# Kernel tuning notes

Hardware: AMD Instinct MI355X
Metric: run time of the kernel (lower is better)

## Reference

```python
import jax, jax.numpy as jnp
import numpy as np

TOPK = 2
ALPHA_AUX = 0.02

def setup_inputs() -> dict:
    key = jax.random.key(0)
    ks = jax.random.split(key, 6)
    B, T, D, E, H = 2, 2048, 1024, 16, 1536
    s_in = 1.0 / np.sqrt(D)
    s_h = 1.0 / np.sqrt(H)
    return {
        "x": jax.random.normal(ks[0], (B, T, D), dtype=jnp.float32),
        "router_w": jax.random.normal(ks[1], (E, D), dtype=jnp.float32) * s_in,
        "w1": jax.random.normal(ks[2], (E, H, D), dtype=jnp.float32) * s_in,
        "b1": jax.random.normal(ks[3], (E, H), dtype=jnp.float32) * 0.01,
        "w2": jax.random.normal(ks[4], (E, D, H), dtype=jnp.float32) * s_h,
        "b2": jax.random.normal(ks[5], (E, D), dtype=jnp.float32) * 0.01,
    }

def reference(x, router_w, w1, b1, w2, b2):
    B, T, D = x.shape
    E = router_w.shape[0]
    N = B * T
    x_flat = x.reshape(N, D)

    # Router: top-k logits -> softmax gates -> dense dispatch matrix [N, E]
    logits = x_flat @ router_w.T                      # [N, E]
    vals, idx = jax.lax.top_k(logits, TOPK)           # [N, K]
    gate = jax.nn.softmax(vals, axis=-1)              # [N, K]
    rows = jnp.arange(N)[:, None]
    dispatch = jnp.zeros((N, E), dtype=x.dtype).at[rows, idx].set(gate)

    # Expert MLPs computed densely over all experts; gate==0 masks unselected,
    # reproducing the gather-MLP-scatter math exactly.
    h = jnp.einsum('nd,ehd->neh', x_flat, w1) + b1    # [N, E, H]
    h = jax.nn.gelu(h, approximate=True)              # tanh GELU
    y = jnp.einsum('neh,edh->ned', h, w2) + b2        # [N, E, D]
    out = jnp.einsum('ne,ned->nd', dispatch, y).reshape(B, T, D)

    # Auxiliary load-balancing loss
    tok_per_expert = (dispatch > 0).sum(0).astype(jnp.float32)  # [E]
    f_i = tok_per_expert / tok_per_expert.sum()
    m_i = dispatch.sum(0) / jnp.clip(tok_per_expert, 1.0, None)
    aux_loss = ALPHA_AUX * (f_i * m_i).mean()
    return out, aux_loss
```

## Files before the change

kernel.cpp:

```cpp
#include <hip/hip_runtime.h>
#include <hip/hip_bf16.h>
#include <math.h>

#define N_TOK 4096
#define DIM   1024
#define NEXP  16
#define HID   1536
#define TOPK2 2
#define NASSIGN (N_TOK * TOPK2)

#define MAX_ITEMS 80

typedef __attribute__((ext_vector_type(8))) short short8;
typedef __attribute__((ext_vector_type(4))) float floatx4;
typedef unsigned short u16;

#define GLOAD_LDS16(gp, lp)                                                     \
    __builtin_amdgcn_global_load_lds(                                           \
        (const __attribute__((address_space(1))) unsigned int*)(gp),            \
        (__attribute__((address_space(3))) unsigned int*)(lp), 16, 0, 0)

__global__ void cvt_kernel(const float* __restrict__ src, u16* __restrict__ dst, int n4) {
    int i = blockIdx.x * 256 + threadIdx.x;
    if (i >= n4) return;
    float4 v = ((const float4*)src)[i];
    __hip_bfloat16 a = __float2bfloat16(v.x), b = __float2bfloat16(v.y);
    __hip_bfloat16 c = __float2bfloat16(v.z), d = __float2bfloat16(v.w);
    ushort4 o;
    o.x = *(u16*)&a; o.y = *(u16*)&b; o.z = *(u16*)&c; o.w = *(u16*)&d;
    ((ushort4*)dst)[i] = o;
}

__global__ __launch_bounds__(256)
void logits_topk_kernel(const float* __restrict__ x, const float* __restrict__ rw,
                        int* __restrict__ idx, float* __restrict__ gate) {
    int tb = blockIdx.x * 16;
    __shared__ float xs[16][68];
    __shared__ float rs[16][68];
    __shared__ float lg[16][17];

    int tid = threadIdx.x;
    int t = tid >> 4, e = tid & 15;
    int srow = tid >> 4, scol = (tid & 15) * 4;

    float acc = 0.f;
    for (int k0 = 0; k0 < DIM; k0 += 64) {
        *(float4*)&xs[srow][scol] = *(const float4*)&x[(size_t)(tb + srow) * DIM + k0 + scol];
        *(float4*)&rs[srow][scol] = *(const float4*)&rw[(size_t)srow * DIM + k0 + scol];
        __syncthreads();
        const float2* xp = (const float2*)xs[t];
        const float2* rp = (const float2*)rs[e];
        #pragma unroll
        for (int k = 0; k < 32; k++) {
            float2 a = xp[k], b = rp[k];
            acc = fmaf(a.x, b.x, acc);
            acc = fmaf(a.y, b.y, acc);
        }
        __syncthreads();
    }
    lg[t][e] = acc;
    __syncthreads();

    if (tid < 16) {
        int n = tb + tid;
        float v0 = -3.402823466e+38f, v1 = -3.402823466e+38f;
        int i0 = 0, i1 = 0;
        #pragma unroll
        for (int ee = 0; ee < NEXP; ee++) {
            float v = lg[tid][ee];
            if (v > v0) { v1 = v0; i1 = i0; v0 = v; i0 = ee; }
            else if (v > v1) { v1 = v; i1 = ee; }
        }
        float e1 = expf(v1 - v0);
        float inv = 1.f / (1.f + e1);
        idx[2 * n] = i0; idx[2 * n + 1] = i1;
        gate[2 * n] = inv; gate[2 * n + 1] = e1 * inv;
    }
}

__global__ __launch_bounds__(256)
void plan_kernel(const int* __restrict__ idx, const float* __restrict__ gate,
                 int* __restrict__ offsets, int* __restrict__ tlist,
                 int* __restrict__ wl, int* __restrict__ wcount,
                 float* __restrict__ aux_out) {
    __shared__ int cnt_s[16];
    __shared__ float gs_s[16];
    __shared__ int pos_s[16];
    __shared__ int offs_s[17];
    int tid = threadIdx.x;
    if (tid < 16) { cnt_s[tid] = 0; gs_s[tid] = 0.f; pos_s[tid] = 0; }
    __syncthreads();
    for (int i = tid; i < NASSIGN; i += 256) {
        int e = idx[i];
        atomicAdd(&cnt_s[e], 1);
        atomicAdd(&gs_s[e], gate[i]);
    }
    __syncthreads();
    if (tid == 0) {
        int acc = 0;
        for (int e = 0; e < NEXP; e++) { offs_s[e] = acc; acc += cnt_s[e]; }
        offs_s[NEXP] = acc;
        float tot = (float)acc;
        float s = 0.f;
        for (int e = 0; e < NEXP; e++) {
            float c = (float)cnt_s[e];
            s += (c / tot) * (gs_s[e] / fmaxf(c, 1.f));
        }
        *aux_out = 0.02f * (s / (float)NEXP);
        int m = 0;
        for (int e = 0; e < NEXP; e++) {
            int nt = (cnt_s[e] + 127) >> 7;
            for (int rt = 0; rt < nt; rt++) wl[m++] = (e << 8) | rt;
        }
        *wcount = m;
    }
    __syncthreads();
    if (tid < 17) offsets[tid] = offs_s[tid];
    for (int i = tid; i < NASSIGN; i += 256) {
        int e = idx[i];
        int p = atomicAdd(&pos_s[e], 1);
        tlist[offs_s[e] + p] = i;
    }
}

__device__ __forceinline__ float gelu_tanh(float v) {
    float v3 = v * v * v;
    float t = tanhf(0.7978845608028654f * (v + 0.044715f * v3));
    return 0.5f * v * (1.f + t);
}


__global__ __launch_bounds__(256)
void gemm1_kernel(const u16* __restrict__ xb, const u16* __restrict__ w1b,
                  const float* __restrict__ b1,
                  const int* __restrict__ offsets, const int* __restrict__ tlist,
                  const int* __restrict__ wl, const int* __restrict__ wcount,
                  u16* __restrict__ h_bf) {
    int bid = blockIdx.x;
    int item = bid / 12;
    if (item >= *wcount) return;
    int colt = bid - item * 12;
    int w = wl[item];
    int e = w >> 8, rt = w & 255;
    int beg = offsets[e], ne = offsets[e + 1] - beg;
    int row0 = rt * 128, col0 = colt * 128;

    __shared__ u16 As[128 * 32];
    __shared__ u16 Bs[128 * 32];

    int tid = threadIdx.x;
    int wave = tid >> 6, lane = tid & 63;
    int wm = wave & 1, wn = wave >> 1;

    int koff = (((lane & 3) ^ ((lane >> 3) & 3)) * 8);
    const u16* aptr[2];
    const u16* bptr[2];
    #pragma unroll
    for (int q = 0; q < 2; q++) {
        int lrow = wave * 32 + q * 16 + (lane >> 2);
        int gi = beg + row0 + lrow;
        int gi2 = (row0 + lrow < ne) ? gi : beg;
        int tok = tlist[gi2] >> 1;
        aptr[q] = xb + (size_t)tok * DIM + koff;
        int n = col0 + lrow;
        bptr[q] = w1b + (size_t)(e * HID + n) * DIM + koff;
    }

    int rchunk = (((lane >> 4) ^ ((lane >> 1) & 3)) * 8);

    floatx4 acc[4][4] = {};
    for (int k0 = 0; k0 < DIM; k0 += 32) {
        #pragma unroll
        for (int q = 0; q < 2; q++) {
            GLOAD_LDS16(aptr[q] + k0, &As[(wave * 32 + q * 16) * 32]);
            GLOAD_LDS16(bptr[q] + k0, &Bs[(wave * 32 + q * 16) * 32]);
        }
        __syncthreads();
        short8 af[4], bf_[4];
        #pragma unroll
        for (int mi = 0; mi < 4; mi++)
            af[mi] = *(const short8*)&As[(wm * 64 + mi * 16 + (lane & 15)) * 32 + rchunk];
        #pragma unroll
        for (int nj = 0; nj < 4; nj++)
            bf_[nj] = *(const short8*)&Bs[(wn * 64 + nj * 16 + (lane & 15)) * 32 + rchunk];
        #pragma unroll
        for (int mi = 0; mi < 4; mi++)
            #pragma unroll
            for (int nj = 0; nj < 4; nj++)
                acc[mi][nj] = __builtin_amdgcn_mfma_f32_16x16x32_bf16(af[mi], bf_[nj], acc[mi][nj], 0, 0, 0);
        __syncthreads();
    }

    #pragma unroll
    for (int mi = 0; mi < 4; mi++) {
        #pragma unroll
        for (int r = 0; r < 4; r++) {
            int lrow = wm * 64 + mi * 16 + (lane >> 4) * 4 + r;
            if (row0 + lrow >= ne) continue;
            size_t orow = (size_t)(beg + row0 + lrow);
            #pragma unroll
            for (int nj = 0; nj < 4; nj++) {
                int col = col0 + wn * 64 + nj * 16 + (lane & 15);
                float v = acc[mi][nj][r] + b1[e * HID + col];
                __hip_bfloat16 hb = __float2bfloat16(gelu_tanh(v));
                h_bf[orow * HID + col] = *(u16*)&hb;
            }
        }
    }
}

__global__ __launch_bounds__(256)
void gemm2_kernel(const u16* __restrict__ h_bf, const u16* __restrict__ w2b,
                  const float* __restrict__ b2,
                  const int* __restrict__ offsets, const int* __restrict__ tlist,
                  const int* __restrict__ wl, const int* __restrict__ wcount,
                  const float* __restrict__ gate, float* __restrict__ out) {
    int bid = blockIdx.x;
    int item = bid >> 3;
    if (item >= *wcount) return;
    int colt = bid & 7;
    int w = wl[item];
    int e = w >> 8, rt = w & 255;
    int beg = offsets[e], ne = offsets[e + 1] - beg;
    int row0 = rt * 128, col0 = colt * 128;

    __shared__ u16 As[128 * 32];
    __shared__ u16 Bs[128 * 32];

    int tid = threadIdx.x;
    int wave = tid >> 6, lane = tid & 63;
    int wm = wave & 1, wn = wave >> 1;

    int koff = (((lane & 3) ^ ((lane >> 3) & 3)) * 8);
    const u16* aptr[2];
    const u16* bptr[2];
    #pragma unroll
    for (int q = 0; q < 2; q++) {
        int lrow = wave * 32 + q * 16 + (lane >> 2);
        int gi = beg + row0 + lrow;
        int gi2 = (row0 + lrow < ne) ? gi : beg;
        aptr[q] = h_bf + (size_t)gi2 * HID + koff;
        int n = col0 + lrow;
        bptr[q] = w2b + (size_t)(e * DIM + n) * HID + koff;
    }

    int rchunk = (((lane >> 4) ^ ((lane >> 1) & 3)) * 8);

    floatx4 acc[4][4] = {};
    for (int k0 = 0; k0 < HID; k0 += 32) {
        #pragma unroll
        for (int q = 0; q < 2; q++) {
            GLOAD_LDS16(aptr[q] + k0, &As[(wave * 32 + q * 16) * 32]);
            GLOAD_LDS16(bptr[q] + k0, &Bs[(wave * 32 + q * 16) * 32]);
        }
        __syncthreads();
        short8 af[4], bf_[4];
        #pragma unroll
        for (int mi = 0; mi < 4; mi++)
            af[mi] = *(const short8*)&As[(wm * 64 + mi * 16 + (lane & 15)) * 32 + rchunk];
        #pragma unroll
        for (int nj = 0; nj < 4; nj++)
            bf_[nj] = *(const short8*)&Bs[(wn * 64 + nj * 16 + (lane & 15)) * 32 + rchunk];
        #pragma unroll
        for (int mi = 0; mi < 4; mi++)
            #pragma unroll
            for (int nj = 0; nj < 4; nj++)
                acc[mi][nj] = __builtin_amdgcn_mfma_f32_16x16x32_bf16(af[mi], bf_[nj], acc[mi][nj], 0, 0, 0);
        __syncthreads();
    }

    #pragma unroll
    for (int mi = 0; mi < 4; mi++) {
        #pragma unroll
        for (int r = 0; r < 4; r++) {
            int lrow = wm * 64 + mi * 16 + (lane >> 4) * 4 + r;
            if (row0 + lrow >= ne) continue;
            int t = tlist[beg + row0 + lrow];
            float g = gate[t];
            int tok = t >> 1;
            #pragma unroll
            for (int nj = 0; nj < 4; nj++) {
                int col = col0 + wn * 64 + nj * 16 + (lane & 15);
                float v = g * (acc[mi][nj][r] + b2[e * DIM + col]);
                atomicAdd(&out[(size_t)tok * DIM + col], v);
            }
        }
    }
}

extern "C" void kernel_launch(void* const* d_in, const int* in_sizes, int n_in,
                              void* d_out, int out_size, void* d_ws, size_t ws_size,
                              hipStream_t stream) {
    const float* x  = (const float*)d_in[0];
    const float* rw = (const float*)d_in[1];
    const float* w1 = (const float*)d_in[2];
    const float* b1 = (const float*)d_in[3];
    const float* w2 = (const float*)d_in[4];
    const float* b2 = (const float*)d_in[5];
    float* out = (float*)d_out;

    char* ws = (char*)d_ws;
    int*   offsets = (int*)(ws + 192);
    int*   wcount  = (int*)(ws + 384);
    int*   wl      = (int*)(ws + 512);
    int*   idx     = (int*)(ws + 4096);
    float* gate    = (float*)(ws + 4096 + 4 * NASSIGN);
    int*   tlist   = (int*)(ws + 4096 + 8 * NASSIGN);
    u16*   x_bf    = (u16*)(ws + (128 << 10));
    u16*   h_bf    = x_bf + (size_t)N_TOK * DIM;
    u16*   w_bf    = h_bf + (size_t)NASSIGN * HID;

    hipMemsetAsync(d_out, 0, (size_t)out_size * 4, stream);

    cvt_kernel<<<(N_TOK * DIM / 4 + 255) / 256, 256, 0, stream>>>(x, x_bf, N_TOK * DIM / 4);
    cvt_kernel<<<(NEXP * HID * DIM / 4 + 255) / 256, 256, 0, stream>>>(w1, w_bf, NEXP * HID * DIM / 4);

    logits_topk_kernel<<<N_TOK / 16, 256, 0, stream>>>(x, rw, idx, gate);
    plan_kernel<<<1, 256, 0, stream>>>(idx, gate, offsets, tlist, wl, wcount,
                                       out + (size_t)N_TOK * DIM);

    gemm1_kernel<<<MAX_ITEMS * 12, 256, 0, stream>>>(
        x_bf, w_bf, b1, offsets, tlist, wl, wcount, h_bf);

    cvt_kernel<<<(NEXP * DIM * HID / 4 + 255) / 256, 256, 0, stream>>>(w2, w_bf, NEXP * DIM * HID / 4);

    gemm2_kernel<<<MAX_ITEMS * 8, 256, 0, stream>>>(
        h_bf, w_bf, b2, offsets, tlist, wl, wcount, gate, out);
}
```

Before: 457.1 us.

## Double K-tile depth to 64 and split GEMM2 over K in two halves

Both expert GEMMs now stage 64-wide K slices in LDS with a new XOR swizzle, which halves the number of barrier pairs per output tile and issues two MFMA groups per sync. GEMM2 also splits its K dimension across two blocks that both accumulate into the output with atomics, with only the first half adding the bias. This doubles GEMM2 block count for better occupancy and load balance, in exchange for twice the atomic traffic on the output and more LDS per block.

New measurement: 490.7 us. 7.4% more time.

```diff
diff --git a/kernel.cpp b/kernel.cpp
--- a/kernel.cpp
+++ b/kernel.cpp
@@ -145,49 +145,53 @@
     int beg = offsets[e], ne = offsets[e + 1] - beg;
     int row0 = rt * 128, col0 = colt * 128;
 
-    __shared__ u16 As[128 * 32];
-    __shared__ u16 Bs[128 * 32];
+    __shared__ u16 As[128 * 64];
+    __shared__ u16 Bs[128 * 64];
 
     int tid = threadIdx.x;
     int wave = tid >> 6, lane = tid & 63;
     int wm = wave & 1, wn = wave >> 1;
 
-    int koff = (((lane & 3) ^ ((lane >> 3) & 3)) * 8);
-    const u16* aptr[2];
-    const u16* bptr[2];
+    int koff = ((lane & 7) ^ (lane >> 3)) * 8;
+    const u16* aptr[4];
+    const u16* bptr[4];
     #pragma unroll
-    for (int q = 0; q < 2; q++) {
-        int lrow = wave * 32 + q * 16 + (lane >> 2);
-        int gi = beg + row0 + lrow;
-        int gi2 = (row0 + lrow < ne) ? gi : beg;
+    for (int q = 0; q < 4; q++) {
+        int lrow = wave * 32 + q * 8 + (lane >> 3);
+        int gi2 = (row0 + lrow < ne) ? (beg + row0 + lrow) : beg;
         int tok = tlist[gi2] >> 1;
         aptr[q] = xb + (size_t)tok * DIM + koff;
-        int n = col0 + lrow;
-        bptr[q] = w1b + (size_t)(e * HID + n) * DIM + koff;
-    }
-
-    int rchunk = (((lane >> 4) ^ ((lane >> 1) & 3)) * 8);
+        bptr[q] = w1b + (size_t)(e * HID + col0 + lrow) * DIM + koff;
+    }
+
+    int rc[2];
+    rc[0] = (((lane >> 4) ^ (lane & 7)) * 8);
+    rc[1] = (((4 + (lane >> 4)) ^ (lane & 7)) * 8);
 
     floatx4 acc[4][4] = {};
-    for (int k0 = 0; k0 < DIM; k0 += 32) {
-        #pragma unroll
-        for (int q = 0; q < 2; q++) {
-            GLOAD_LDS16(aptr[q] + k0, &As[(wave * 32 + q * 16) * 32]);
-            GLOAD_LDS16(bptr[q] + k0, &Bs[(wave * 32 + q * 16) * 32]);
-        }
-        __syncthreads();
-        short8 af[4], bf_[4];
-        #pragma unroll
-        for (int mi = 0; mi < 4; mi++)
-            af[mi] = *(const short8*)&As[(wm * 64 + mi * 16 + (lane & 15)) * 32 + rchunk];
-        #pragma unroll
-        for (int nj = 0; nj < 4; nj++)
-            bf_[nj] = *(const short8*)&Bs[(wn * 64 + nj * 16 + (lane & 15)) * 32 + rchunk];
-        #pragma unroll
-        for (int mi = 0; mi < 4; mi++)
+    for (int k0 = 0; k0 < DIM; k0 += 64) {
+        #pragma unroll
+        for (int q = 0; q < 4; q++)
+            GLOAD_LDS16(aptr[q] + k0, &As[(wave * 32 + q * 8) * 64]);
+        #pragma unroll
+        for (int q = 0; q < 4; q++)
+            GLOAD_LDS16(bptr[q] + k0, &Bs[(wave * 32 + q * 8) * 64]);
+        __syncthreads();
+        #pragma unroll
+        for (int g = 0; g < 2; g++) {
+            short8 af[4], bf_[4];
+            #pragma unroll
+            for (int mi = 0; mi < 4; mi++)
+                af[mi] = *(const short8*)&As[(wm * 64 + mi * 16 + (lane & 15)) * 64 + rc[g]];
             #pragma unroll
             for (int nj = 0; nj < 4; nj++)
-                acc[mi][nj] = __builtin_amdgcn_mfma_f32_16x16x32_bf16(af[mi], bf_[nj], acc[mi][nj], 0, 0, 0);
+                bf_[nj] = *(const short8*)&Bs[(wn * 64 + nj * 16 + (lane & 15)) * 64 + rc[g]];
+            #pragma unroll
+            for (int mi = 0; mi < 4; mi++)
+                #pragma unroll
+                for (int nj = 0; nj < 4; nj++)
+                    acc[mi][nj] = __builtin_amdgcn_mfma_f32_16x16x32_bf16(af[mi], bf_[nj], acc[mi][nj], 0, 0, 0);
+        }
         __syncthreads();
     }
 
@@ -216,56 +220,62 @@
                   const int* __restrict__ wl, const int* __restrict__ wcount,
                   const float* __restrict__ gate, float* __restrict__ out) {
     int bid = blockIdx.x;
-    int item = bid >> 3;
+    int item = bid >> 4;
     if (item >= *wcount) return;
-    int colt = bid & 7;
+    int colt = (bid >> 1) & 7;
+    int ks = bid & 1;
     int w = wl[item];
     int e = w >> 8, rt = w & 255;
     int beg = offsets[e], ne = offsets[e + 1] - beg;
     int row0 = rt * 128, col0 = colt * 128;
-
-    __shared__ u16 As[128 * 32];
-    __shared__ u16 Bs[128 * 32];
+    int kbeg = ks * (HID / 2);
+
+    __shared__ u16 As[128 * 64];
+    __shared__ u16 Bs[128 * 64];
 
     int tid = threadIdx.x;
     int wave = tid >> 6, lane = tid & 63;
     int wm = wave & 1, wn = wave >> 1;
 
-    int koff = (((lane & 3) ^ ((lane >> 3) & 3)) * 8);
-    const u16* aptr[2];
-    const u16* bptr[2];
+    int koff = ((lane & 7) ^ (lane >> 3)) * 8;
+    const u16* aptr[4];
+    const u16* bptr[4];
     #pragma unroll
-    for (int q = 0; q < 2; q++) {
-        int lrow = wave * 32 + q * 16 + (lane >> 2);
-        int gi = beg + row0 + lrow;
-        int gi2 = (row0 + lrow < ne) ? gi : beg;
-        aptr[q] = h_bf + (size_t)gi2 * HID + koff;
-        int n = col0 + lrow;
-        bptr[q] = w2b + (size_t)(e * DIM + n) * HID + koff;
-    }
-
-    int rchunk = (((lane >> 4) ^ ((lane >> 1) & 3)) * 8);
+    for (int q = 0; q < 4; q++) {
+        int lrow = wave * 32 + q * 8 + (lane >> 3);
+        int gi2 = (row0 + lrow < ne) ? (beg + row0 + lrow) : beg;
+        aptr[q] = h_bf + (size_t)gi2 * HID + kbeg + koff;
+        bptr[q] = w2b + (size_t)(e * DIM + col0 + lrow) * HID + kbeg + koff;
+    }
+
+    int rc[2];
+    rc[0] = (((lane >> 4) ^ (lane & 7)) * 8);
+    rc[1] = (((4 + (lane >> 4)) ^ (lane & 7)) * 8);
 
     floatx4 acc[4][4] = {};
-    for (int k0 = 0; k0 < HID; k0 += 32) {
-        #pragma unroll
-        for (int q = 0; q < 2; q++) {
-            GLOAD_LDS16(aptr[q] + k0, &As[(wave * 32 + q * 16) * 32]);
-            GLOAD_LDS16(bptr[q] + k0, &Bs[(wave * 32 + q * 16) * 32]);
-        }
-        __syncthreads();
-        short8 af[4], bf_[4];
-        #pragma unroll
-        for (int mi = 0; mi < 4; mi++)
-            af[mi] = *(const short8*)&As[(wm * 64 + mi * 16 + (lane & 15)) * 32 + rchunk];
-        #pragma unroll
-        for (int nj = 0; nj < 4; nj++)
-            bf_[nj] = *(const short8*)&Bs[(wn * 64 + nj * 16 + (lane & 15)) * 32 + rchunk];
-        #pragma unroll
-        for (int mi = 0; mi < 4; mi++)
+    for (int k0 = 0; k0 < HID / 2; k0 += 64) {
+        #pragma unroll
+        for (int q = 0; q < 4; q++)
+            GLOAD_LDS16(aptr[q] + k0, &As[(wave * 32 + q * 8) * 64]);
+        #pragma unroll
+        for (int q = 0; q < 4; q++)
+            GLOAD_LDS16(bptr[q] + k0, &Bs[(wave * 32 + q * 8) * 64]);
+        __syncthreads();
+        #pragma unroll
+        for (int g = 0; g < 2; g++) {
+            short8 af[4], bf_[4];
+            #pragma unroll
+            for (int mi = 0; mi < 4; mi++)
+                af[mi] = *(const short8*)&As[(wm * 64 + mi * 16 + (lane & 15)) * 64 + rc[g]];
             #pragma unroll
             for (int nj = 0; nj < 4; nj++)
-                acc[mi][nj] = __builtin_amdgcn_mfma_f32_16x16x32_bf16(af[mi], bf_[nj], acc[mi][nj], 0, 0, 0);
+                bf_[nj] = *(const short8*)&Bs[(wn * 64 + nj * 16 + (lane & 15)) * 64 + rc[g]];
+            #pragma unroll
+            for (int mi = 0; mi < 4; mi++)
+                #pragma unroll
+                for (int nj = 0; nj < 4; nj++)
+                    acc[mi][nj] = __builtin_amdgcn_mfma_f32_16x16x32_bf16(af[mi], bf_[nj], acc[mi][nj], 0, 0, 0);
+        }
         __syncthreads();
     }
 
@@ -281,8 +291,9 @@
             #pragma unroll
             for (int nj = 0; nj < 4; nj++) {
                 int col = col0 + wn * 64 + nj * 16 + (lane & 15);
-                float v = g * (acc[mi][nj][r] + b2[e * DIM + col]);
-                atomicAdd(&out[(size_t)tok * DIM + col], v);
+                float v = acc[mi][nj][r];
+                if (ks == 0) v += b2[e * DIM + col];
+                atomicAdd(&out[(size_t)tok * DIM + col], g * v);
             }
         }
     }
@@ -324,6 +335,6 @@
 
     cvt_kernel<<<(NEXP * DIM * HID / 4 + 255) / 256, 256, 0, stream>>>(w2, w_bf, NEXP * DIM * HID / 4);
 
-    gemm2_kernel<<<MAX_ITEMS * 8, 256, 0, stream>>>(
+    gemm2_kernel<<<MAX_ITEMS * 16, 256, 0, stream>>>(
         h_bf, w_bf, b2, offsets, tlist, wl, wcount, gate, out);
 }
```
